# Kernel tuning notes

Measured on AMD Instinct MI355X. Metric: run time of the kernel, lower is better.

## Reference

```python
import jax, jax.numpy as jnp
import numpy as np

VOC_SIZE = 65536
DIM = 256
BATCH = 4096
NUM_TOPK = 32
TEMPERATURE = 1.0


def setup_inputs() -> dict:
    key = jax.random.key(0)
    ks = jax.random.split(key, 8)
    scale = 1.0 / np.sqrt(DIM)
    return {
        "x": jax.random.normal(ks[0], (BATCH, DIM), dtype=jnp.float32),
        "codebook": jax.random.normal(ks[1], (VOC_SIZE, DIM), dtype=jnp.float32),
        "Wq": jax.random.normal(ks[2], (DIM, DIM), dtype=jnp.float32) * scale,
        "bq": jax.random.normal(ks[3], (DIM,), dtype=jnp.float32) * scale,
        "Wk": jax.random.normal(ks[4], (DIM, DIM), dtype=jnp.float32) * scale,
        "bk": jax.random.normal(ks[5], (DIM,), dtype=jnp.float32) * scale,
        "Wv": jax.random.normal(ks[6], (DIM, DIM), dtype=jnp.float32) * scale,
        "bv": jax.random.normal(ks[7], (DIM,), dtype=jnp.float32) * scale,
    }


def reference(x, codebook, Wq, bq, Wk, bk, Wv, bv):
    # Linear projections (torch Linear: y = x @ W.T + b)
    q = x @ Wq.T + bq                      # [B, D]
    k = codebook @ Wk.T + bk               # [V, D]
    v = codebook @ Wv.T + bv               # [V, D]

    dots = jnp.einsum('bd,kd->bk', q, k)   # [B, V]
    top_value, top_ind = jax.lax.top_k(dots, NUM_TOPK)  # sorted desc, like torch.topk

    # mask everything strictly below the k-th largest score
    vk = top_value[:, -1:]                 # [B, 1]
    mask_value = -jnp.finfo(dots.dtype).max
    dots_masked = jnp.where(dots < vk, mask_value, dots)

    attn = jax.nn.softmax(dots_masked / TEMPERATURE, axis=-1)
    out = jnp.einsum('bk,kd->bd', attn, v)  # [B, D]
    return (out, top_value, top_ind, dots_masked)
```

## Files before the change

kernel.cpp:

```cpp
#include <hip/hip_runtime.h>
#include <float.h>
#include <math.h>

#define DIMK 256
#define VOC 65536
#define BATCH 4096
#define NTOP 32

#define MASKV -3.3895313892515355e+38f

typedef __bf16 bf16x8 __attribute__((ext_vector_type(8)));
typedef float f32x4 __attribute__((ext_vector_type(4)));
typedef float f4 __attribute__((ext_vector_type(4)));
typedef unsigned int u32x4 __attribute__((ext_vector_type(4)));
typedef unsigned int u32x2 __attribute__((ext_vector_type(2)));

__device__ __forceinline__ ushort f2bf(float f) {
    unsigned u = __float_as_uint(f);
    u = (u + 0x7fffu + ((u >> 16) & 1u)) >> 16;
    return (ushort)u;
}
__device__ __forceinline__ float bflo(unsigned u) { return __uint_as_float(u << 16); }
__device__ __forceinline__ float bfhi(unsigned u) { return __uint_as_float(u & 0xFFFF0000u); }

#define GLOAD_LDS16(gsrc, ldst)                                                \
    __builtin_amdgcn_global_load_lds(                                          \
        (const __attribute__((address_space(1))) unsigned int*)(gsrc),         \
        (__attribute__((address_space(3))) unsigned int*)(ldst), 16, 0, 0)

__global__ __launch_bounds__(256) void gemm_nt(
    const float* __restrict__ A, const float* __restrict__ B,
    const float* __restrict__ bias, float* __restrict__ C, int N, int swap, int obf16)
{
    __shared__ float As[16][132];
    __shared__ float Bs[16][132];
    const int bn = swap ? blockIdx.y : blockIdx.x;
    const int bm = swap ? blockIdx.x : blockIdx.y;
    const int tid = threadIdx.x;
    const int tx = tid & 15, ty = tid >> 4;
    const float* Ab = A + (size_t)bm * 128 * DIMK;
    const float* Bb = B + (size_t)bn * 128 * DIMK;

    float acc[2][2][4][4];
#pragma unroll
    for (int rg = 0; rg < 2; rg++)
#pragma unroll
        for (int cg = 0; cg < 2; cg++)
#pragma unroll
            for (int r = 0; r < 4; r++)
#pragma unroll
                for (int c = 0; c < 4; c++) acc[rg][cg][r][c] = 0.f;

    for (int k0 = 0; k0 < DIMK; k0 += 16) {
#pragma unroll
        for (int r = 0; r < 2; ++r) {
            int i = tid + r * 256;
            int row = i >> 2;
            int kc = (i & 3) << 2;
            const float4 va = *(const float4*)(Ab + (size_t)row * DIMK + k0 + kc);
            As[kc + 0][row] = va.x; As[kc + 1][row] = va.y;
            As[kc + 2][row] = va.z; As[kc + 3][row] = va.w;
            const float4 vb = *(const float4*)(Bb + (size_t)row * DIMK + k0 + kc);
            Bs[kc + 0][row] = vb.x; Bs[kc + 1][row] = vb.y;
            Bs[kc + 2][row] = vb.z; Bs[kc + 3][row] = vb.w;
        }
        __syncthreads();
#pragma unroll
        for (int k = 0; k < 16; ++k) {
            const float4 a0 = *(const float4*)&As[k][ty * 4];
            const float4 a1 = *(const float4*)&As[k][64 + ty * 4];
            const float4 b0 = *(const float4*)&Bs[k][tx * 4];
            const float4 b1 = *(const float4*)&Bs[k][64 + tx * 4];
            const float ar[2][4] = { {a0.x, a0.y, a0.z, a0.w}, {a1.x, a1.y, a1.z, a1.w} };
            const float bc[2][4] = { {b0.x, b0.y, b0.z, b0.w}, {b1.x, b1.y, b1.z, b1.w} };
#pragma unroll
            for (int rg = 0; rg < 2; rg++)
#pragma unroll
                for (int cg = 0; cg < 2; cg++)
#pragma unroll
                    for (int r = 0; r < 4; r++)
#pragma unroll
                        for (int c = 0; c < 4; c++)
                            acc[rg][cg][r][c] = fmaf(ar[rg][r], bc[cg][c], acc[rg][cg][r][c]);
        }
        __syncthreads();
    }

#pragma unroll
    for (int rg = 0; rg < 2; rg++)
#pragma unroll
        for (int r = 0; r < 4; r++) {
            size_t row = (size_t)bm * 128 + rg * 64 + ty * 4 + r;
#pragma unroll
            for (int cg = 0; cg < 2; cg++) {
                int col = bn * 128 + cg * 64 + tx * 4;
                float4 o;
                o.x = acc[rg][cg][r][0]; o.y = acc[rg][cg][r][1];
                o.z = acc[rg][cg][r][2]; o.w = acc[rg][cg][r][3];
                if (bias) {
                    o.x += bias[col + 0]; o.y += bias[col + 1];
                    o.z += bias[col + 2]; o.w += bias[col + 3];
                }
                if (obf16) {
                    ushort4 ob;
                    ob.x = f2bf(o.x); ob.y = f2bf(o.y);
                    ob.z = f2bf(o.z); ob.w = f2bf(o.w);
                    *(ushort4*)((ushort*)C + row * (size_t)N + col) = ob;
                } else {
                    *(float4*)(C + row * (size_t)N + col) = o;
                }
            }
        }
}

__global__ __launch_bounds__(256) void dots_mfma(
    const ushort* __restrict__ Qb,
    const ushort* __restrict__ Kb,
    ushort* __restrict__ Db)
{
    __shared__ __align__(16) ushort As[2][128 * 32];
    __shared__ __align__(16) ushort Bs[2][128 * 32];
    const int bm = blockIdx.x;
    const int bn = blockIdx.y;
    const int tid = threadIdx.x;
    const int w = tid >> 6, l = tid & 63;
    const int wm = w >> 1, wn = w & 1;

    const ushort* Ab = Qb + (size_t)bm * 128 * DIMK;
    const ushort* Bb = Kb + (size_t)bn * 128 * DIMK;

    const int sr = l >> 2;
    const int sc = (l & 3) ^ ((l >> 3) & 3);
    const int fr = l & 15;
    const int pc = (l >> 4) ^ ((fr >> 1) & 3);

    const int slab0 = w * 2, slab1 = w * 2 + 1;
    const ushort* gA0 = Ab + (size_t)(slab0 * 16 + sr) * DIMK + sc * 8;
    const ushort* gA1 = Ab + (size_t)(slab1 * 16 + sr) * DIMK + sc * 8;
    const ushort* gB0 = Bb + (size_t)(slab0 * 16 + sr) * DIMK + sc * 8;
    const ushort* gB1 = Bb + (size_t)(slab1 * 16 + sr) * DIMK + sc * 8;

#define STAGE_DM(buf, kk) do {                                   \
        GLOAD_LDS16(gA0 + (kk), &As[buf][slab0 * 512]);          \
        GLOAD_LDS16(gB0 + (kk), &Bs[buf][slab0 * 512]);          \
        GLOAD_LDS16(gA1 + (kk), &As[buf][slab1 * 512]);          \
        GLOAD_LDS16(gB1 + (kk), &Bs[buf][slab1 * 512]);          \
    } while (0)

    f32x4 acc[4][4];
    const f32x4 zero = {0.f, 0.f, 0.f, 0.f};
#pragma unroll
    for (int i = 0; i < 4; ++i)
#pragma unroll
        for (int j = 0; j < 4; ++j) acc[i][j] = zero;

    STAGE_DM(0, 0);
    asm volatile("s_waitcnt vmcnt(0)" ::: "memory");
    __builtin_amdgcn_s_barrier();
    asm volatile("" ::: "memory");

#pragma unroll
    for (int t = 0; t < 8; ++t) {
        const int cur = t & 1;
        if (t < 7) STAGE_DM(cur ^ 1, (t + 1) * 32);

        uint4 a4[4], b4[4];
#pragma unroll
        for (int f = 0; f < 4; ++f) {
            a4[f] = *(const uint4*)(&As[cur][(wm * 64 + f * 16 + fr) * 32 + pc * 8]);
            b4[f] = *(const uint4*)(&Bs[cur][(wn * 64 + f * 16 + fr) * 32 + pc * 8]);
        }
#pragma unroll
        for (int i = 0; i < 4; ++i)
#pragma unroll
            for (int j = 0; j < 4; ++j)
                acc[i][j] = __builtin_amdgcn_mfma_f32_16x16x32_bf16(
                    __builtin_bit_cast(bf16x8, b4[i]),
                    __builtin_bit_cast(bf16x8, a4[j]),
                    acc[i][j], 0, 0, 0);

        if (t < 7) {
            asm volatile("s_waitcnt vmcnt(0)" ::: "memory");
            __builtin_amdgcn_s_barrier();
            asm volatile("" ::: "memory");
        }
    }
#undef STAGE_DM

    const int kq = (l >> 4) * 4;
    const int qc = l & 15;
#pragma unroll
    for (int i = 0; i < 4; ++i)
#pragma unroll
        for (int j = 0; j < 4; ++j) {
            const size_t q = (size_t)(bm * 128 + wm * 64 + j * 16 + qc);
            const size_t k = (size_t)(bn * 128 + wn * 64 + i * 16 + kq);
            unsigned p0, p1;
            asm("v_cvt_pk_bf16_f32 %0, %1, %2" : "=v"(p0) : "v"(acc[i][j][0]), "v"(acc[i][j][1]));
            asm("v_cvt_pk_bf16_f32 %0, %1, %2" : "=v"(p1) : "v"(acc[i][j][2]), "v"(acc[i][j][3]));
            u32x2 pv; pv.x = p0; pv.y = p1;
            *(u32x2*)(Db + q * (size_t)(2 * VOC) + k) = pv;
        }
}

__device__ __forceinline__ bool pair_gt(float av, int ai, float bv, int bi) {
    return (av > bv) || (av == bv && ai < bi);
}

__global__ __launch_bounds__(256) void scan_select(
    const float* __restrict__ dots, float* __restrict__ topv, int* __restrict__ topi)
{
    const int row = blockIdx.x;
    const int tid = threadIdx.x;
    const int w = tid >> 6, l = tid & 63;
    const u32x4* rb = (const u32x4*)(dots + ((size_t)row << 16));

    __shared__ float s_wt[4];
    __shared__ int   s_cnt;
    __shared__ float cv[2048];
    __shared__ int   ci[2048];

    float gm[32];
    float tmax = -FLT_MAX;
#pragma unroll
    for (int it = 0; it < 4; ++it) {
        u32x4 uu[8];
#pragma unroll
        for (int b = 0; b < 8; ++b)
            uu[b] = rb[it * 2048 + b * 256 + tid];
#pragma unroll
        for (int b = 0; b < 8; ++b) {
            const u32x4 u = uu[b];
            const float m = fmaxf(
                fmaxf(fmaxf(bflo(u.x), bfhi(u.x)), fmaxf(bflo(u.y), bfhi(u.y))),
                fmaxf(fmaxf(bflo(u.z), bfhi(u.z)), fmaxf(bflo(u.w), bfhi(u.w))));
            gm[it * 8 + b] = m;
            tmax = fmaxf(tmax, m);
        }
    }

    float cur = tmax, Tw = -FLT_MAX;
#pragma unroll
    for (int r = 0; r < 8; ++r) {
        float m = cur;
#pragma unroll
        for (int off = 32; off; off >>= 1) m = fmaxf(m, __shfl_xor(m, off));
        Tw = m;
        cur = (cur == m) ? -FLT_MAX : cur;
    }
    if (l == 0) s_wt[w] = Tw;
    if (tid == 0) s_cnt = 0;
    __syncthreads();
    const float Tb = fminf(fminf(s_wt[0], s_wt[1]), fminf(s_wt[2], s_wt[3]));

#pragma unroll
    for (int it = 0; it < 4; ++it)
#pragma unroll
        for (int b = 0; b < 8; ++b) {
            if (gm[it * 8 + b] >= Tb) {
                const int gidx = it * 2048 + b * 256 + tid;
                const u32x4 u = rb[gidx];
                const float vv[8] = { bflo(u.x), bfhi(u.x), bflo(u.y), bfhi(u.y),
                                      bflo(u.z), bfhi(u.z), bflo(u.w), bfhi(u.w) };
#pragma unroll
                for (int j = 0; j < 8; ++j) {
                    if (vv[j] >= Tb) {
                        const int p = atomicAdd(&s_cnt, 1);
                        if (p < 2048) { cv[p] = vv[j]; ci[p] = gidx * 8 + j; }
                    }
                }
            }
        }
    __syncthreads();
    const int n = (s_cnt < 2048) ? s_cnt : 2048;

    if (w != 0) return;

    for (int r = 0; r < NTOP; ++r) {
        float bv_ = -FLT_MAX; int bi_ = 0x7fffffff;
        for (int p = l; p < n; p += 64) {
            const float vv = cv[p]; const int ii = ci[p];
            if (pair_gt(vv, ii, bv_, bi_)) { bv_ = vv; bi_ = ii; }
        }
#pragma unroll
        for (int off = 32; off; off >>= 1) {
            const float ov = __shfl_xor(bv_, off);
            const int   oi = __shfl_xor(bi_, off);
            if (pair_gt(ov, oi, bv_, bi_)) { bv_ = ov; bi_ = oi; }
        }
        if (l == 0) {
            topv[(size_t)row * NTOP + r] = bv_;
            topi[(size_t)row * NTOP + r] = bi_;
        }
        for (int p = l; p < n; p += 64)
            if (ci[p] == bi_) { cv[p] = -FLT_MAX; ci[p] = 0x7fffffff; }
    }
}

__global__ __launch_bounds__(256) void fill_all(float* __restrict__ dots)
{
    const f4 mv4 = { MASKV, MASKV, MASKV, MASKV };
    f4* p = (f4*)dots;
    const size_t n = (size_t)BATCH * VOC / 4;
    const size_t stride = (size_t)gridDim.x * 256;
    for (size_t i = (size_t)blockIdx.x * 256 + threadIdx.x; i < n; i += stride)
        __builtin_nontemporal_store(mv4, p + i);
}

__global__ __launch_bounds__(256) void tail_k(
    float* __restrict__ dots, const float* __restrict__ topv, const int* __restrict__ topi,
    const float* __restrict__ codebook, const float* __restrict__ Wv,
    const float* __restrict__ bvec, float* __restrict__ out)
{
    const int row = blockIdx.x;
    const int tid = threadIdx.x;
    float* rp = dots + ((size_t)row << 16);

    __shared__ float s_t32v[NTOP];
    __shared__ int   s_t32i[NTOP];
    __shared__ float s_attn[NTOP];
    __shared__ float s_inv;
    __shared__ float s_wc[256];

    if (tid < NTOP) {
        const float tv = topv[(size_t)row * NTOP + tid];
        const int   ti = topi[(size_t)row * NTOP + tid];
        s_t32v[tid] = tv; s_t32i[tid] = ti;
        rp[ti] = tv;
    }
    __syncthreads();

    if (tid < NTOP) s_attn[tid] = expf(s_t32v[tid] - s_t32v[0]);
    __syncthreads();
    if (tid == 0) {
        float s = 0.f;
        for (int j = 0; j < NTOP; j++) s += s_attn[j];
        s_inv = 1.0f / s;
    }
    __syncthreads();

    float wc = 0.f;
    for (int j = 0; j < NTOP; j++)
        wc = fmaf(s_attn[j], codebook[(size_t)s_t32i[j] * DIMK + tid], wc);
    wc *= s_inv;

    s_wc[tid] = wc;
    __syncthreads();

    float acc = bvec[tid];
    const float4* wr = (const float4*)(Wv + (size_t)tid * DIMK);
#pragma unroll 4
    for (int e = 0; e < DIMK / 4; e++) {
        float4 wv4 = wr[e];
        acc = fmaf(wv4.x, s_wc[4 * e + 0], acc);
        acc = fmaf(wv4.y, s_wc[4 * e + 1], acc);
        acc = fmaf(wv4.z, s_wc[4 * e + 2], acc);
        acc = fmaf(wv4.w, s_wc[4 * e + 3], acc);
    }
    out[(size_t)row * DIMK + tid] = acc;
}

extern "C" void kernel_launch(void* const* d_in, const int* in_sizes, int n_in,
                              void* d_out, int out_size, void* d_ws, size_t ws_size,
                              hipStream_t stream) {
    const float* x        = (const float*)d_in[0];
    const float* codebook = (const float*)d_in[1];
    const float* Wq       = (const float*)d_in[2];
    const float* bq       = (const float*)d_in[3];
    const float* Wk       = (const float*)d_in[4];
    const float* bk       = (const float*)d_in[5];
    const float* Wv       = (const float*)d_in[6];
    const float* bv       = (const float*)d_in[7];

    float* out_f = (float*)d_out;
    float* topv  = out_f + (size_t)BATCH * DIMK;
    int*   topi  = (int*)(topv + (size_t)BATCH * NTOP);
    float* dotsm = (float*)(topi + (size_t)BATCH * NTOP);

    ushort* kb16 = (ushort*)d_ws;
    ushort* qb16 = kb16 + (size_t)VOC * DIMK;

    gemm_nt<<<dim3(DIMK / 128, BATCH / 128), 256, 0, stream>>>(x, Wq, bq, (float*)qb16, DIMK, 0, 1);
    gemm_nt<<<dim3(DIMK / 128, VOC / 128), 256, 0, stream>>>(codebook, Wk, bk, (float*)kb16, DIMK, 0, 1);
    dots_mfma<<<dim3(BATCH / 128, VOC / 128), 256, 0, stream>>>(qb16, kb16, (ushort*)dotsm);
    scan_select<<<BATCH, 256, 0, stream>>>(dotsm, topv, topi);
    fill_all<<<2048, 256, 0, stream>>>(dotsm);
    tail_k<<<BATCH, 256, 0, stream>>>(dotsm, topv, topi, codebook, Wv, bv, out_f);
}
```

Before: 1.876 ms.

## Emit per-tile row maxima from dots GEMM and fuse mask fill into tail

The dots GEMM epilogue now writes a per-row maximum for each 64-column tile into a small workspace array. The selection kernel reads these maxima instead of streaming the whole bf16 row to find thresholds, and then rereads only the tiles that can hold top-k candidates. The separate fill kernel is removed and the mask fill is done per row inside the tail kernel before the top-k values are scattered back. This trades a full extra pass over the dots buffer plus one launch for extra epilogue work and shuffles in the GEMM, and the candidate buffer shrinks to 1024 entries.

New measurement: 1.702 ms. 9.2% less time.

```diff
diff --git a/kernel.cpp b/kernel.cpp
--- a/kernel.cpp
+++ b/kernel.cpp
@@ -116,7 +116,8 @@
 __global__ __launch_bounds__(256) void dots_mfma(
     const ushort* __restrict__ Qb,
     const ushort* __restrict__ Kb,
-    ushort* __restrict__ Db)
+    ushort* __restrict__ Db,
+    float* __restrict__ Rm)
 {
     __shared__ __align__(16) ushort As[2][128 * 32];
     __shared__ __align__(16) ushort Bs[2][128 * 32];
@@ -201,6 +202,21 @@
             u32x2 pv; pv.x = p0; pv.y = p1;
             *(u32x2*)(Db + q * (size_t)(2 * VOC) + k) = pv;
         }
+
+#pragma unroll
+    for (int j = 0; j < 4; ++j) {
+        float m = -FLT_MAX;
+#pragma unroll
+        for (int i = 0; i < 4; ++i)
+#pragma unroll
+            for (int r = 0; r < 4; ++r) m = fmaxf(m, acc[i][j][r]);
+        m = fmaxf(m, __shfl_xor(m, 16));
+        m = fmaxf(m, __shfl_xor(m, 32));
+        if (l < 16) {
+            const size_t qrow = (size_t)(bm * 128 + wm * 64 + j * 16 + l);
+            Rm[qrow * 1024 + (bn * 2 + wn)] = bflo((unsigned)f2bf(m));
+        }
+    }
 }
 
 __device__ __forceinline__ bool pair_gt(float av, int ai, float bv, int bi) {
@@ -208,36 +224,20 @@
 }
 
 __global__ __launch_bounds__(256) void scan_select(
-    const float* __restrict__ dots, float* __restrict__ topv, int* __restrict__ topi)
+    const float* __restrict__ dots, const float* __restrict__ Rm,
+    float* __restrict__ topv, int* __restrict__ topi)
 {
     const int row = blockIdx.x;
     const int tid = threadIdx.x;
     const int w = tid >> 6, l = tid & 63;
-    const u32x4* rb = (const u32x4*)(dots + ((size_t)row << 16));
 
     __shared__ float s_wt[4];
     __shared__ int   s_cnt;
-    __shared__ float cv[2048];
-    __shared__ int   ci[2048];
-
-    float gm[32];
-    float tmax = -FLT_MAX;
-#pragma unroll
-    for (int it = 0; it < 4; ++it) {
-        u32x4 uu[8];
-#pragma unroll
-        for (int b = 0; b < 8; ++b)
-            uu[b] = rb[it * 2048 + b * 256 + tid];
-#pragma unroll
-        for (int b = 0; b < 8; ++b) {
-            const u32x4 u = uu[b];
-            const float m = fmaxf(
-                fmaxf(fmaxf(bflo(u.x), bfhi(u.x)), fmaxf(bflo(u.y), bfhi(u.y))),
-                fmaxf(fmaxf(bflo(u.z), bfhi(u.z)), fmaxf(bflo(u.w), bfhi(u.w))));
-            gm[it * 8 + b] = m;
-            tmax = fmaxf(tmax, m);
-        }
-    }
+    __shared__ float cv[1024];
+    __shared__ int   ci[1024];
+
+    const f4 rv = *(const f4*)(Rm + (size_t)row * 1024 + tid * 4);
+    const float tmax = fmaxf(fmaxf(rv.x, rv.y), fmaxf(rv.z, rv.w));
 
     float cur = tmax, Tw = -FLT_MAX;
 #pragma unroll
@@ -253,26 +253,28 @@
     __syncthreads();
     const float Tb = fminf(fminf(s_wt[0], s_wt[1]), fminf(s_wt[2], s_wt[3]));
 
-#pragma unroll
-    for (int it = 0; it < 4; ++it)
-#pragma unroll
-        for (int b = 0; b < 8; ++b) {
-            if (gm[it * 8 + b] >= Tb) {
-                const int gidx = it * 2048 + b * 256 + tid;
-                const u32x4 u = rb[gidx];
+    const u32x4* rb = (const u32x4*)(dots + ((size_t)row << 16));
+#pragma unroll
+    for (int c = 0; c < 4; ++c) {
+        if (rv[c] >= Tb) {
+            const int kt = tid * 4 + c;
+#pragma unroll
+            for (int g = 0; g < 8; ++g) {
+                const u32x4 u = rb[kt * 8 + g];
                 const float vv[8] = { bflo(u.x), bfhi(u.x), bflo(u.y), bfhi(u.y),
                                       bflo(u.z), bfhi(u.z), bflo(u.w), bfhi(u.w) };
 #pragma unroll
                 for (int j = 0; j < 8; ++j) {
                     if (vv[j] >= Tb) {
                         const int p = atomicAdd(&s_cnt, 1);
-                        if (p < 2048) { cv[p] = vv[j]; ci[p] = gidx * 8 + j; }
+                        if (p < 1024) { cv[p] = vv[j]; ci[p] = kt * 64 + g * 8 + j; }
                     }
                 }
             }
         }
-    __syncthreads();
-    const int n = (s_cnt < 2048) ? s_cnt : 2048;
+    }
+    __syncthreads();
+    const int n = (s_cnt < 1024) ? s_cnt : 1024;
 
     if (w != 0) return;
 
@@ -295,16 +297,6 @@
         for (int p = l; p < n; p += 64)
             if (ci[p] == bi_) { cv[p] = -FLT_MAX; ci[p] = 0x7fffffff; }
     }
-}
-
-__global__ __launch_bounds__(256) void fill_all(float* __restrict__ dots)
-{
-    const f4 mv4 = { MASKV, MASKV, MASKV, MASKV };
-    f4* p = (f4*)dots;
-    const size_t n = (size_t)BATCH * VOC / 4;
-    const size_t stride = (size_t)gridDim.x * 256;
-    for (size_t i = (size_t)blockIdx.x * 256 + threadIdx.x; i < n; i += stride)
-        __builtin_nontemporal_store(mv4, p + i);
 }
 
 __global__ __launch_bounds__(256) void tail_k(
@@ -323,12 +315,18 @@
     __shared__ float s_wc[256];
 
     if (tid < NTOP) {
-        const float tv = topv[(size_t)row * NTOP + tid];
-        const int   ti = topi[(size_t)row * NTOP + tid];
-        s_t32v[tid] = tv; s_t32i[tid] = ti;
-        rp[ti] = tv;
-    }
-    __syncthreads();
+        s_t32v[tid] = topv[(size_t)row * NTOP + tid];
+        s_t32i[tid] = topi[(size_t)row * NTOP + tid];
+    }
+    __syncthreads();
+
+    {
+        const f4 mv4 = { MASKV, MASKV, MASKV, MASKV };
+        f4* rp4 = (f4*)rp;
+#pragma unroll 8
+        for (int k = 0; k < 64; ++k)
+            __builtin_nontemporal_store(mv4, rp4 + tid + k * 256);
+    }
 
     if (tid < NTOP) s_attn[tid] = expf(s_t32v[tid] - s_t32v[0]);
     __syncthreads();
@@ -337,6 +335,7 @@
         for (int j = 0; j < NTOP; j++) s += s_attn[j];
         s_inv = 1.0f / s;
     }
+    if (tid < NTOP) rp[s_t32i[tid]] = s_t32v[tid];
     __syncthreads();
 
     float wc = 0.f;
@@ -379,11 +378,11 @@
 
     ushort* kb16 = (ushort*)d_ws;
     ushort* qb16 = kb16 + (size_t)VOC * DIMK;
+    float*  Rm   = (float*)(qb16 + (size_t)BATCH * DIMK);
 
     gemm_nt<<<dim3(DIMK / 128, BATCH / 128), 256, 0, stream>>>(x, Wq, bq, (float*)qb16, DIMK, 0, 1);
     gemm_nt<<<dim3(DIMK / 128, VOC / 128), 256, 0, stream>>>(codebook, Wk, bk, (float*)kb16, DIMK, 0, 1);
-    dots_mfma<<<dim3(BATCH / 128, VOC / 128), 256, 0, stream>>>(qb16, kb16, (ushort*)dotsm);
-    scan_select<<<BATCH, 256, 0, stream>>>(dotsm, topv, topi);
-    fill_all<<<2048, 256, 0, stream>>>(dotsm);
+    dots_mfma<<<dim3(BATCH / 128, VOC / 128), 256, 0, stream>>>(qb16, kb16, (ushort*)dotsm, Rm);
+    scan_select<<<BATCH, 256, 0, stream>>>(dotsm, Rm, topv, topi);
     tail_k<<<BATCH, 256, 0, stream>>>(dotsm, topv, topi, codebook, Wv, bv, out_f);
 }
```
